# Optimization experiments

Hardware: AMD Instinct MI355X
Metric: run time of the kernel (lower is better)

The kernel has to match this reference:

```python
import jax, jax.numpy as jnp
import numpy as np

C_M, C_Z, C = 256, 128, 32
N_SEQ, N_RES = 128, 256


def setup_inputs() -> dict:
    key = jax.random.key(0)
    ks = jax.random.split(key, 8)
    m = jax.random.normal(ks[0], (N_SEQ, N_RES, C_M), dtype=jnp.float32)
    gamma = jnp.ones((C_M,), dtype=jnp.float32)
    beta = jnp.zeros((C_M,), dtype=jnp.float32)
    s = 1.0 / np.sqrt(C_M)
    W1 = jax.random.normal(ks[1], (C_M, C), dtype=jnp.float32) * s
    b1 = jax.random.normal(ks[2], (C,), dtype=jnp.float32) * 0.01
    W2 = jax.random.normal(ks[3], (C_M, C), dtype=jnp.float32) * s
    b2 = jax.random.normal(ks[4], (C,), dtype=jnp.float32) * 0.01
    Wout = jax.random.normal(ks[5], (C * C, C_Z), dtype=jnp.float32) / np.sqrt(C * C)
    bout = jax.random.normal(ks[6], (C_Z,), dtype=jnp.float32) * 0.01
    return {"m": m, "gamma": gamma, "beta": beta, "W1": W1, "b1": b1,
            "W2": W2, "b2": b2, "Wout": Wout, "bout": bout}


def _layernorm(x, gamma, beta, eps=1e-5):
    mu = jnp.mean(x, axis=-1, keepdims=True)
    var = jnp.var(x, axis=-1, keepdims=True)
    return (x - mu) * jax.lax.rsqrt(var + eps) * gamma + beta


def reference(m, gamma, beta, W1, b1, W2, b2, Wout, bout):
    n_seq = m.shape[-3]
    mn = _layernorm(m, gamma, beta)              # (s, i, c_m)
    a = mn @ W1 + b1                              # (s, i, c)
    b = mn @ W2 + b2                              # (s, j, c)
    o = jnp.einsum('sic,sjk->ijck', a, b)        # (i, j, c, c)
    o = o.reshape(o.shape[0], o.shape[1], -1)    # (i, j, c*c)
    z = (o @ Wout + bout) / n_seq                # (i, j, c_z)
    return z
```

## Files before the change

kernel.cpp:

```cpp
#include <hip/hip_runtime.h>
#include <hip/hip_bf16.h>

typedef __attribute__((ext_vector_type(8))) short short8;
typedef __attribute__((ext_vector_type(4))) short short4v;
typedef __attribute__((ext_vector_type(4))) float f32x4;

#define WS_A   0
#define WS_B   (8192 * 128 * 2)
#define WS_WT  (2 * 8192 * 128 * 2)
#define WS_W12 (WS_WT + 128 * 1024 * 2)

static __device__ __forceinline__ short f2bf(float x) {
    __hip_bfloat16 h = __float2bfloat16(x);
    return *reinterpret_cast<short*>(&h);
}

typedef __attribute__((address_space(3))) unsigned int lds_u32;
typedef const __attribute__((address_space(1))) unsigned int glb_u32;
static __device__ __forceinline__ void stage16(const void* g, void* l) {
    __builtin_amdgcn_global_load_lds((glb_u32*)g, (lds_u32*)l, 16, 0, 0);
}

__global__ __launch_bounds__(256) void k_prep(const float* __restrict__ Wout,
                                              const float* __restrict__ W1,
                                              const float* __restrict__ W2,
                                              __hip_bfloat16* __restrict__ WoutT,
                                              __hip_bfloat16* __restrict__ W12bf) {
    int idx = blockIdx.x * 256 + threadIdx.x;
    if (blockIdx.x < 512) {
        int z = idx >> 10, ck = idx & 1023;
        WoutT[idx] = __float2bfloat16(Wout[ck * 128 + z]);
    } else {
        idx -= 512 * 256;
        int c = idx >> 8, d = idx & 255;
        W12bf[idx] = __float2bfloat16(c < 32 ? W1[d * 32 + c] : W2[d * 32 + (c - 32)]);
    }
}

__global__ __launch_bounds__(256) void k_lnproj(const float* __restrict__ mm,
                                                const float* __restrict__ gamma,
                                                const float* __restrict__ beta,
                                                const float* __restrict__ b1,
                                                const float* __restrict__ b2,
                                                const __hip_bfloat16* __restrict__ W12bf,
                                                __hip_bfloat16* __restrict__ Ap,
                                                __hip_bfloat16* __restrict__ Bp) {
    __shared__ char sMN[4][8192];
    const int lane = threadIdx.x & 63;
    const int wid  = threadIdx.x >> 6;
    const int gw   = blockIdx.x * 4 + wid;
    const int i_   = gw & 255;
    const int sb   = (gw >> 8) * 16;

    float4 g4  = *(const float4*)&gamma[lane * 4];
    float4 be4 = *(const float4*)&beta[lane * 4];
    char* my = sMN[wid];

    #pragma unroll
    for (int rr = 0; rr < 16; rr++) {
        float4 x = *(const float4*)&mm[((size_t)(sb + rr) * 256 + i_) * 256 + lane * 4];
        float s  = x.x + x.y + x.z + x.w;
        float ss = x.x * x.x + x.y * x.y + x.z * x.z + x.w * x.w;
        #pragma unroll
        for (int off = 32; off; off >>= 1) {
            s  += __shfl_xor(s, off);
            ss += __shfl_xor(ss, off);
        }
        float mu  = s * (1.f / 256.f);
        float var = ss * (1.f / 256.f) - mu * mu;
        float rs  = rsqrtf(var + 1e-5f);
        short4v v;
        v.x = f2bf((x.x - mu) * rs * g4.x + be4.x);
        v.y = f2bf((x.y - mu) * rs * g4.y + be4.y);
        v.z = f2bf((x.z - mu) * rs * g4.z + be4.z);
        v.w = f2bf((x.w - mu) * rs * g4.w + be4.w);
        *(short4v*)(my + rr * 512 + ((lane * 8) ^ ((rr & 7) << 4))) = v;
    }

    const short* wt12 = (const short*)W12bf;
    const int g = lane >> 4, r16 = lane & 15;

    f32x4 acc[4];
    #pragma unroll
    for (int nf = 0; nf < 4; nf++) {
        int col = nf * 16 + r16;
        float bv = (col < 32) ? b1[col] : b2[col - 32];
        acc[nf] = (f32x4){bv, bv, bv, bv};
    }
    #pragma unroll
    for (int ks = 0; ks < 8; ks++) {
        int L = ks * 64 + g * 16;
        short8 af = *(const short8*)(my + r16 * 512 + (L ^ ((r16 & 7) << 4)));
        #pragma unroll
        for (int nf = 0; nf < 4; nf++) {
            short8 bfv = *(const short8*)&wt12[(nf * 16 + r16) * 256 + ks * 32 + g * 8];
            acc[nf] = __builtin_amdgcn_mfma_f32_16x16x32_bf16(af, bfv, acc[nf], 0, 0, 0);
        }
    }
    #pragma unroll
    for (int nf = 0; nf < 4; nf++) {
        int col = nf * 16 + r16;
        short* Out = (short*)((col < 32) ? Ap : Bp);
        int cr = col & 31;
        short4v v;
        v.x = f2bf(acc[nf][0]); v.y = f2bf(acc[nf][1]);
        v.z = f2bf(acc[nf][2]); v.w = f2bf(acc[nf][3]);
        *(short4v*)&Out[(i_ * 32 + cr) * 128 + sb + g * 4] = v;
    }
}

extern __shared__ char lds[];

__global__ __launch_bounds__(512, 2) void k_gemm4(const __hip_bfloat16* __restrict__ Apb,
                                                  const __hip_bfloat16* __restrict__ Bpb,
                                                  const __hip_bfloat16* __restrict__ WoutT,
                                                  const float* __restrict__ bout,
                                                  float* __restrict__ out) {
    const int t = threadIdx.x, lane = t & 63, wid = t >> 6;
    const int g = lane >> 4, r16 = lane & 15;
    const int wr = wid >> 2, wc = wid & 3;
    const int bi = blockIdx.x >> 5, bj = blockIdx.x & 31;

    const short* gA = (const short*)Apb + (size_t)bi * 256 * 128;
    const short* gB = (const short*)Bpb + (size_t)bj * 256 * 128;

    const int srow8 = lane >> 3;
    const int sgran = (lane & 7) ^ srow8;
    #pragma unroll
    for (int kh = 0; kh < 2; kh++) {
        #pragma unroll
        for (int rd = 0; rd < 4; rd++) {
            const int row = rd * 64 + wid * 8 + srow8;
            stage16(gB + row * 128 + kh * 64 + sgran * 8,
                    lds + kh * 65536 + rd * 8192 + wid * 1024);
            stage16(gA + row * 128 + kh * 64 + sgran * 8,
                    lds + kh * 65536 + 32768 + rd * 8192 + wid * 1024);
        }
    }

    asm volatile("s_waitcnt vmcnt(8)" ::: "memory");
    __builtin_amdgcn_s_barrier();

    f32x4 acc[8][4];
    #pragma unroll
    for (int mf = 0; mf < 8; mf++)
        #pragma unroll
        for (int nf = 0; nf < 4; nf++)
            acc[mf][nf] = (f32x4){0.f, 0.f, 0.f, 0.f};

    #pragma unroll
    for (int kh = 0; kh < 2; kh++) {
        if (kh) {
            asm volatile("s_waitcnt vmcnt(0)" ::: "memory");
            __builtin_amdgcn_s_barrier();
        }
        const char* sBb = lds + kh * 65536;
        const char* sAb = lds + kh * 65536 + 32768;
        #pragma unroll
        for (int ksl = 0; ksl < 2; ksl++) {
            short8 af[8], bfv[4];
            #pragma unroll
            for (int mf = 0; mf < 8; mf++) {
                const int row = wr * 128 + mf * 16 + r16;
                af[mf] = *(const short8*)(sBb + row * 128 + (((ksl * 4 + g) ^ (row & 7)) << 4));
            }
            #pragma unroll
            for (int nf = 0; nf < 4; nf++) {
                const int row = wc * 64 + nf * 16 + r16;
                bfv[nf] = *(const short8*)(sAb + row * 128 + (((ksl * 4 + g) ^ (row & 7)) << 4));
            }
            __builtin_amdgcn_s_setprio(1);
            #pragma unroll
            for (int mf = 0; mf < 8; mf++)
                #pragma unroll
                for (int nf = 0; nf < 4; nf++)
                    acc[mf][nf] = __builtin_amdgcn_mfma_f32_16x16x32_bf16(af[mf], bfv[nf], acc[mf][nf], 0, 0, 0);
            __builtin_amdgcn_s_setprio(0);
        }
    }
    __builtin_amdgcn_s_barrier();

    const int z = wid * 16 + r16;
    const float bv = bout[z];
    f32x4 acc2[4];
    #pragma unroll
    for (int pf = 0; pf < 4; pf++) acc2[pf] = (f32x4){bv, bv, bv, bv};
    const short* wt = (const short*)WoutT;

    #define REPACK(h)                                                                    \
        {                                                                                \
            char* sPh = lds + (h) * 65536;                                               \
            _Pragma("unroll")                                                            \
            for (int nq = 0; nq < 2; nq++) {                                             \
                const int nf = (h) + nq * 2;                                             \
                const int p = (wc * 2 + nq) * 8 + wr * 4;                                \
                _Pragma("unroll")                                                        \
                for (int mf = 0; mf < 8; mf++) {                                         \
                    const int pp = p + (mf >> 1);                                        \
                    const int L = r16 * 64 + (mf & 1) * 32 + g * 8;                      \
                    short4v v;                                                           \
                    v.x = f2bf(acc[mf][nf][0]); v.y = f2bf(acc[mf][nf][1]);              \
                    v.z = f2bf(acc[mf][nf][2]); v.w = f2bf(acc[mf][nf][3]);              \
                    *(short4v*)(sPh + pp * 1024 + (L ^ ((((L >> 7) ^ pp) & 7) << 4))) = v; \
                }                                                                        \
            }                                                                            \
        }

    #define EPI(h)                                                                       \
        {                                                                                \
            const char* sPh = lds + (h) * 65536;                                         \
            _Pragma("unroll 4")                                                          \
            for (int ks = 0; ks < 16; ks++) {                                            \
                short8 wf = *(const short8*)&wt[z * 1024 + (h) * 512 + ks * 32 + g * 8]; \
                _Pragma("unroll")                                                        \
                for (int pf = 0; pf < 4; pf++) {                                         \
                    const int row = pf * 16 + r16;                                       \
                    const int L = ks * 64 + g * 16;                                      \
                    short8 pv = *(const short8*)(sPh + row * 1024 +                      \
                                                 (L ^ ((((L >> 7) ^ row) & 7) << 4)));   \
                    acc2[pf] = __builtin_amdgcn_mfma_f32_16x16x32_bf16(pv, wf, acc2[pf], 0, 0, 0); \
                }                                                                        \
            }                                                                            \
        }

    REPACK(0)
    asm volatile("s_waitcnt lgkmcnt(0)" ::: "memory");
    __builtin_amdgcn_s_barrier();
    REPACK(1)
    EPI(0)
    asm volatile("s_waitcnt lgkmcnt(0)" ::: "memory");
    __builtin_amdgcn_s_barrier();
    EPI(1)

    #pragma unroll
    for (int pf = 0; pf < 4; pf++) {
        #pragma unroll
        for (int reg = 0; reg < 4; reg++) {
            const int p = pf * 16 + g * 4 + reg;
            const int ig = bi * 8 + (p >> 3), jg = bj * 8 + (p & 7);
            out[((size_t)(ig * 256 + jg)) * 128 + z] = acc2[pf][reg] * (1.f / 128.f);
        }
    }
    #undef REPACK
    #undef EPI
}

extern "C" void kernel_launch(void* const* d_in, const int* in_sizes, int n_in,
                              void* d_out, int out_size, void* d_ws, size_t ws_size,
                              hipStream_t stream) {
    const float* mm    = (const float*)d_in[0];
    const float* gamma = (const float*)d_in[1];
    const float* beta  = (const float*)d_in[2];
    const float* W1    = (const float*)d_in[3];
    const float* b1    = (const float*)d_in[4];
    const float* W2    = (const float*)d_in[5];
    const float* b2    = (const float*)d_in[6];
    const float* Wout  = (const float*)d_in[7];
    const float* bout  = (const float*)d_in[8];

    __hip_bfloat16* Ap    = (__hip_bfloat16*)((char*)d_ws + WS_A);
    __hip_bfloat16* Bp    = (__hip_bfloat16*)((char*)d_ws + WS_B);
    __hip_bfloat16* WoutT = (__hip_bfloat16*)((char*)d_ws + WS_WT);
    __hip_bfloat16* W12bf = (__hip_bfloat16*)((char*)d_ws + WS_W12);
    float* out = (float*)d_out;

    (void)hipFuncSetAttribute(reinterpret_cast<const void*>(k_gemm4),
                              hipFuncAttributeMaxDynamicSharedMemorySize, 131072);

    hipLaunchKernelGGL(k_prep, dim3(576), dim3(256), 0, stream, Wout, W1, W2, WoutT, W12bf);
    hipLaunchKernelGGL(k_lnproj, dim3(512), dim3(256), 0, stream,
                       mm, gamma, beta, b1, b2, W12bf, Ap, Bp);
    hipLaunchKernelGGL(k_gemm4, dim3(1024), dim3(512), 131072, stream,
                       Ap, Bp, WoutT, bout, out);
}
```

Baseline: 76.97 us.

## Restructure epilogue GEMM with 32x32 MFMA tiles and split-K reduction across waves

The second GEMM (outer-product tile times Wout) now repacks the whole 64x1024 tile into LDS in one pass instead of two halves. Each wave then computes a 32-row by 64-column output block with 32x32x16 MFMAs over half of K. The two K halves are summed through LDS before the bias is added and the result is stored. This cuts the number of MFMA instructions and the redundant LDS reads per output in the epilogue. In exchange it adds an extra LDS round trip and barrier for the reduction, plus larger accumulator register use.

```diff
diff --git a/kernel.cpp b/kernel.cpp
--- a/kernel.cpp
+++ b/kernel.cpp
@@ -4,6 +4,7 @@
 typedef __attribute__((ext_vector_type(8))) short short8;
 typedef __attribute__((ext_vector_type(4))) short short4v;
 typedef __attribute__((ext_vector_type(4))) float f32x4;
+typedef __attribute__((ext_vector_type(16))) float f32x16;
 
 #define WS_A   0
 #define WS_B   (8192 * 128 * 2)
@@ -111,7 +112,7 @@
 
 extern __shared__ char lds[];
 
-__global__ __launch_bounds__(512, 2) void k_gemm4(const __hip_bfloat16* __restrict__ Apb,
+__global__ __launch_bounds__(512, 2) void k_gemm5(const __hip_bfloat16* __restrict__ Apb,
                                                   const __hip_bfloat16* __restrict__ Bpb,
                                                   const __hip_bfloat16* __restrict__ WoutT,
                                                   const float* __restrict__ bout,
@@ -180,69 +181,85 @@
     }
     __builtin_amdgcn_s_barrier();
 
-    const int z = wid * 16 + r16;
-    const float bv = bout[z];
-    f32x4 acc2[4];
-    #pragma unroll
-    for (int pf = 0; pf < 4; pf++) acc2[pf] = (f32x4){bv, bv, bv, bv};
-    const short* wt = (const short*)WoutT;
-
-    #define REPACK(h)                                                                    \
-        {                                                                                \
-            char* sPh = lds + (h) * 65536;                                               \
-            _Pragma("unroll")                                                            \
-            for (int nq = 0; nq < 2; nq++) {                                             \
-                const int nf = (h) + nq * 2;                                             \
-                const int p = (wc * 2 + nq) * 8 + wr * 4;                                \
-                _Pragma("unroll")                                                        \
-                for (int mf = 0; mf < 8; mf++) {                                         \
-                    const int pp = p + (mf >> 1);                                        \
-                    const int L = r16 * 64 + (mf & 1) * 32 + g * 8;                      \
-                    short4v v;                                                           \
-                    v.x = f2bf(acc[mf][nf][0]); v.y = f2bf(acc[mf][nf][1]);              \
-                    v.z = f2bf(acc[mf][nf][2]); v.w = f2bf(acc[mf][nf][3]);              \
-                    *(short4v*)(sPh + pp * 1024 + (L ^ ((((L >> 7) ^ pp) & 7) << 4))) = v; \
-                }                                                                        \
-            }                                                                            \
-        }
-
-    #define EPI(h)                                                                       \
-        {                                                                                \
-            const char* sPh = lds + (h) * 65536;                                         \
-            _Pragma("unroll 4")                                                          \
-            for (int ks = 0; ks < 16; ks++) {                                            \
-                short8 wf = *(const short8*)&wt[z * 1024 + (h) * 512 + ks * 32 + g * 8]; \
-                _Pragma("unroll")                                                        \
-                for (int pf = 0; pf < 4; pf++) {                                         \
-                    const int row = pf * 16 + r16;                                       \
-                    const int L = ks * 64 + g * 16;                                      \
-                    short8 pv = *(const short8*)(sPh + row * 1024 +                      \
-                                                 (L ^ ((((L >> 7) ^ row) & 7) << 4)));   \
-                    acc2[pf] = __builtin_amdgcn_mfma_f32_16x16x32_bf16(pv, wf, acc2[pf], 0, 0, 0); \
-                }                                                                        \
-            }                                                                            \
-        }
-
-    REPACK(0)
+    char* sP = lds;
+    #pragma unroll
+    for (int nf = 0; nf < 4; nf++) {
+        const int i_loc = wc * 2 + (nf >> 1);
+        #pragma unroll
+        for (int mf = 0; mf < 8; mf++) {
+            const int p  = i_loc * 8 + wr * 4 + (mf >> 1);
+            const int eb = (nf & 1) * 512 + r16 * 32 + (mf & 1) * 16 + g * 4;
+            const int gr = eb >> 3;
+            const int byte = p * 2048 + (((gr ^ (p & 7)) << 4)) + ((eb & 7) << 1);
+            short4v v;
+            v.x = f2bf(acc[mf][nf][0]); v.y = f2bf(acc[mf][nf][1]);
+            v.z = f2bf(acc[mf][nf][2]); v.w = f2bf(acc[mf][nf][3]);
+            *(short4v*)(sP + byte) = v;
+        }
+    }
     asm volatile("s_waitcnt lgkmcnt(0)" ::: "memory");
     __builtin_amdgcn_s_barrier();
-    REPACK(1)
-    EPI(0)
+
+    const int im = wid >> 2, in_ = (wid >> 1) & 1, ik = wid & 1;
+    const int l31 = lane & 31, kg = lane >> 5;
+    const int prow = im * 32 + l31;
+    const char* sProw = sP + prow * 2048;
+    const int rsw = (prow & 7) << 4;
+    const short* wt0 = (const short*)WoutT + (in_ * 64 + l31) * 1024;
+
+    f32x16 e0 = {0,0,0,0,0,0,0,0,0,0,0,0,0,0,0,0};
+    f32x16 e1 = {0,0,0,0,0,0,0,0,0,0,0,0,0,0,0,0};
+    #pragma unroll 8
+    for (int ks = 0; ks < 32; ks++) {
+        const int ckb = ik * 512 + ks * 16 + kg * 8;
+        short8 pa = *(const short8*)(sProw + (((ckb >> 3) << 4) ^ rsw));
+        short8 w0 = *(const short8*)&wt0[ckb];
+        short8 w1 = *(const short8*)&wt0[32 * 1024 + ckb];
+        e0 = __builtin_amdgcn_mfma_f32_32x32x16_bf16(pa, w0, e0, 0, 0, 0);
+        e1 = __builtin_amdgcn_mfma_f32_32x32x16_bf16(pa, w1, e1, 0, 0, 0);
+    }
+
     asm volatile("s_waitcnt lgkmcnt(0)" ::: "memory");
     __builtin_amdgcn_s_barrier();
-    EPI(1)
-
-    #pragma unroll
-    for (int pf = 0; pf < 4; pf++) {
-        #pragma unroll
-        for (int reg = 0; reg < 4; reg++) {
-            const int p = pf * 16 + g * 4 + reg;
-            const int ig = bi * 8 + (p >> 3), jg = bj * 8 + (p & 7);
-            out[((size_t)(ig * 256 + jg)) * 128 + z] = acc2[pf][reg] * (1.f / 128.f);
-        }
-    }
-    #undef REPACK
-    #undef EPI
+
+    const int q = wid >> 1;
+    char* rbuf = sP + q * 8192 + lane * 128;
+    if (ik) {
+        #pragma unroll
+        for (int c = 0; c < 4; c++) {
+            f32x4 v0 = {e0[c*4+0], e0[c*4+1], e0[c*4+2], e0[c*4+3]};
+            f32x4 v1 = {e1[c*4+0], e1[c*4+1], e1[c*4+2], e1[c*4+3]};
+            *(f32x4*)(rbuf + (((c    ) ^ (lane & 7)) << 4)) = v0;
+            *(f32x4*)(rbuf + (((c + 4) ^ (lane & 7)) << 4)) = v1;
+        }
+    }
+    asm volatile("s_waitcnt lgkmcnt(0)" ::: "memory");
+    __builtin_amdgcn_s_barrier();
+
+    if (!ik) {
+        float eS[32];
+        #pragma unroll
+        for (int c = 0; c < 4; c++) {
+            f32x4 v0 = *(const f32x4*)(rbuf + (((c    ) ^ (lane & 7)) << 4));
+            f32x4 v1 = *(const f32x4*)(rbuf + (((c + 4) ^ (lane & 7)) << 4));
+            #pragma unroll
+            for (int j = 0; j < 4; j++) {
+                eS[c * 4 + j]      = e0[c * 4 + j] + v0[j];
+                eS[16 + c * 4 + j] = e1[c * 4 + j] + v1[j];
+            }
+        }
+        #pragma unroll
+        for (int nf = 0; nf < 2; nf++) {
+            const int z  = in_ * 64 + nf * 32 + l31;
+            const float bv = bout[z];
+            #pragma unroll
+            for (int r = 0; r < 16; r++) {
+                const int p  = im * 32 + (r & 3) + 8 * (r >> 2) + 4 * kg;
+                const int ig = bi * 8 + (p >> 3), jg = bj * 8 + (p & 7);
+                out[((size_t)(ig * 256 + jg)) * 128 + z] = (eS[nf * 16 + r] + bv) * (1.f / 128.f);
+            }
+        }
+    }
 }
 
 extern "C" void kernel_launch(void* const* d_in, const int* in_sizes, int n_in,
@@ -264,12 +281,12 @@
     __hip_bfloat16* W12bf = (__hip_bfloat16*)((char*)d_ws + WS_W12);
     float* out = (float*)d_out;
 
-    (void)hipFuncSetAttribute(reinterpret_cast<const void*>(k_gemm4),
+    (void)hipFuncSetAttribute(reinterpret_cast<const void*>(k_gemm5),
                               hipFuncAttributeMaxDynamicSharedMemorySize, 131072);
 
     hipLaunchKernelGGL(k_prep, dim3(576), dim3(256), 0, stream, Wout, W1, W2, WoutT, W12bf);
     hipLaunchKernelGGL(k_lnproj, dim3(512), dim3(256), 0, stream,
                        mm, gamma, beta, b1, b2, W12bf, Ap, Bp);
-    hipLaunchKernelGGL(k_gemm4, dim3(1024), dim3(512), 131072, stream,
+    hipLaunchKernelGGL(k_gemm5, dim3(1024), dim3(512), 131072, stream,
                        Ap, Bp, WoutT, bout, out);
 }
```

Measured after the change: 116.9 us. 51.9% more time.
